# Performance work log

Hardware: AMD Instinct MI355X
Metric: run time of the kernel (lower is better)

## Reference

```python
import jax, jax.numpy as jnp
import numpy as np

B, S, D, H = 2, 2048, 1024, 16
DK = D // H


def setup_inputs() -> dict:
    key = jax.random.key(0)
    ks = jax.random.split(key, 7)
    scale = 1.0 / np.sqrt(D)
    return {
        "q": jax.random.normal(ks[0], (B, S, D), dtype=jnp.float32),
        "k": jax.random.normal(ks[1], (B, S, D), dtype=jnp.float32),
        "v": jax.random.normal(ks[2], (B, S, D), dtype=jnp.float32),
        "mask": jnp.ones((B, 1, 1, S), dtype=jnp.int32),
        "Wq": (jax.random.normal(ks[3], (D, D), dtype=jnp.float32) * scale),
        "Wk": (jax.random.normal(ks[4], (D, D), dtype=jnp.float32) * scale),
        "Wv": (jax.random.normal(ks[5], (D, D), dtype=jnp.float32) * scale),
        "Wo": (jax.random.normal(ks[6], (D, D), dtype=jnp.float32) * scale),
    }


def reference(q, k, v, mask, Wq, Wk, Wv, Wo):
    # nn.Linear(bias=False): y = x @ W.T
    def split_heads(x):  # [B,S,D] -> [B,H,S,DK]
        return x.reshape(B, S, H, DK).transpose(0, 2, 1, 3)

    qh = split_heads(q @ Wq.T)
    kh = split_heads(k @ Wk.T)
    vh = split_heads(v @ Wv.T)

    scores = jnp.einsum("bhqd,bhkd->bhqk", qh, kh) / jnp.sqrt(
        jnp.asarray(DK, dtype=qh.dtype))
    scores = jnp.where(mask == 0, jnp.asarray(-1e9, dtype=scores.dtype), scores)
    attn = jax.nn.softmax(scores, axis=-1)  # dropout p=0.0 -> identity

    ctx = jnp.einsum("bhqk,bhkd->bhqd", attn, vh)  # [B,H,S,DK]
    ctx = ctx.transpose(0, 2, 1, 3).reshape(B, S, D)
    return ctx @ Wo.T
```

## Files before the change

kernel.cpp:

```cpp
#include <hip/hip_runtime.h>


typedef __bf16 bf16x8 __attribute__((ext_vector_type(8)));
typedef __bf16 bf16x4 __attribute__((ext_vector_type(4)));
typedef float f32x4 __attribute__((ext_vector_type(4)));

#define B_ 2
#define S_ 2048
#define D_ 1024
#define H_ 16
#define DK_ 64
#define QSCALE 0.18033688011112042f

__global__ void detect_dtype(const unsigned int* __restrict__ qw,
                             int* __restrict__ flag) {
  int cnt = 0;
#pragma unroll
  for (int i = 0; i < 4; ++i) {
    unsigned int w = qw[threadIdx.x + 64 * i];
    int e = (w >> 7) & 0xFF;
    cnt += (e >= 100 && e <= 140) ? 1 : 0;
  }
#pragma unroll
  for (int off = 32; off > 0; off >>= 1) cnt += __shfl_down(cnt, off, 64);
  if (threadIdx.x == 0) *flag = (cnt >= 128) ? 0 : 1;
}

__device__ __forceinline__ bf16x8 load8cvt(const void* base, size_t eoff,
                                           bool f32) {
  if (!f32) return *(const bf16x8*)((const __bf16*)base + eoff);
  const float* p = (const float*)base + eoff;
  bf16x8 r;
#pragma unroll
  for (int j = 0; j < 8; ++j) r[j] = (__bf16)p[j];
  return r;
}

__device__ __forceinline__ void async_cp16(const __bf16* g, __bf16* l) {
  __builtin_amdgcn_global_load_lds(
      (const __attribute__((address_space(1))) unsigned int*)g,
      (__attribute__((address_space(3))) unsigned int*)l, 16, 0, 0);
}

template <int TM, int MODE>
__global__ __launch_bounds__(256) void gemmk(
    const void* X0, const void* X1, const void* X2,
    const void* W0, const void* W1, const void* W2,
    void* O0, void* O1, void* O2, const int* __restrict__ dflag) {
  constexpr int Kd = 1024, Nd = 1024;
  constexpr int NI = (TM == 128) ? 4 : 2;
  constexpr int ALOADS = TM / 64;
  const void* X = (blockIdx.z == 0) ? X0 : (blockIdx.z == 1 ? X1 : X2);
  const void* W = (blockIdx.z == 0) ? W0 : (blockIdx.z == 1 ? W1 : W2);
  void* O = (blockIdx.z == 0) ? O0 : (blockIdx.z == 1 ? O1 : O2);
  const bool f32io = (*dflag != 0);

  __shared__ __attribute__((aligned(16))) __bf16 As[TM * 32];
  __shared__ __attribute__((aligned(16))) __bf16 Bs[128 * 32];

  const int m0 = blockIdx.x * TM;
  const int n0 = blockIdx.y * 128;
  const int t = threadIdx.x;
  const int lane = t & 63, wave = t >> 6;
  const int l15 = lane & 15, quad = lane >> 4;
  const int wm = (TM == 128) ? (wave >> 1) * 64 : 0;
  const int wn = (TM == 128) ? (wave & 1) * 64 : wave * 32;

  const __bf16* gA[ALOADS];
  __bf16* ldsA[ALOADS];
#pragma unroll
  for (int i = 0; i < ALOADS; ++i) {
    int c = (wave * ALOADS + i) * 64 + lane;
    int row = c >> 2, j = c & 3;
    int jl = j ^ ((row >> 1) & 3);
    ldsA[i] = &As[(wave * ALOADS + i) * 512];
    if (MODE == 0) {
      gA[i] = (const __bf16*)X + (size_t)(m0 + row) * Kd + jl * 8;
    } else {
      int gm = m0 + row;
      gA[i] = (const __bf16*)X +
              (size_t)(gm >> 11) * (H_ * S_ * DK_) + (size_t)(gm & (S_ - 1)) * DK_ +
              jl * 8;
    }
  }
  const __bf16* gB[2];
  __bf16* ldsB[2];
#pragma unroll
  for (int i = 0; i < 2; ++i) {
    int c = (wave * 2 + i) * 64 + lane;
    int row = c >> 2, j = c & 3;
    int jl = j ^ ((row >> 1) & 3);
    ldsB[i] = &Bs[(wave * 2 + i) * 512];
    gB[i] = (const __bf16*)W + (size_t)(n0 + row) * Kd + jl * 8;
  }

  f32x4 acc[4][NI] = {};

  for (int k0 = 0; k0 < Kd; k0 += 32) {
    __syncthreads();
    if (!f32io) {
      if (MODE == 0) {
#pragma unroll
        for (int i = 0; i < ALOADS; ++i) async_cp16(gA[i] + k0, ldsA[i]);
      } else {
        const size_t koff = (size_t)(k0 >> 6) * (S_ * DK_) + (k0 & 32);
#pragma unroll
        for (int i = 0; i < ALOADS; ++i) async_cp16(gA[i] + koff, ldsA[i]);
      }
#pragma unroll
      for (int i = 0; i < 2; ++i) async_cp16(gB[i] + k0, ldsB[i]);
    } else {
#pragma unroll
      for (int i = 0; i < TM / 64; ++i) {
        int c = t + 256 * i;
        int row = c >> 2, j = c & 3;
        int jl = j ^ ((row >> 1) & 3);
        bf16x8 xv;
        if (MODE == 0) {
          xv = load8cvt(X, (size_t)(m0 + row) * Kd + k0 + jl * 8, true);
        } else {
          int gm = m0 + row, gk = k0 + jl * 8;
          xv = *(const bf16x8*)((const __bf16*)X +
                ((((size_t)(gm >> 11) * H_ + (gk >> 6)) * S_) +
                 (gm & (S_ - 1))) * DK_ + (gk & (DK_ - 1)));
        }
        *(bf16x8*)&As[row * 32 + j * 8] = xv;
      }
#pragma unroll
      for (int i = 0; i < 2; ++i) {
        int c = t + 256 * i;
        int row = c >> 2, j = c & 3;
        int jl = j ^ ((row >> 1) & 3);
        bf16x8 wv = load8cvt(W, (size_t)(n0 + row) * Kd + k0 + jl * 8, true);
        *(bf16x8*)&Bs[row * 32 + j * 8] = wv;
      }
    }
    __syncthreads();

    bf16x8 af[4], bfr[NI];
#pragma unroll
    for (int mi = 0; mi < 4; ++mi) {
      int row = wm + mi * 16 + l15;
      af[mi] = *(const bf16x8*)&As[row * 32 + ((quad ^ ((row >> 1) & 3)) << 3)];
    }
#pragma unroll
    for (int ni = 0; ni < NI; ++ni) {
      int row = wn + ni * 16 + l15;
      bfr[ni] = *(const bf16x8*)&Bs[row * 32 + ((quad ^ ((row >> 1) & 3)) << 3)];
    }
#pragma unroll
    for (int mi = 0; mi < 4; ++mi)
#pragma unroll
      for (int ni = 0; ni < NI; ++ni)
        acc[mi][ni] = __builtin_amdgcn_mfma_f32_16x16x32_bf16(af[mi], bfr[ni],
                                                              acc[mi][ni], 0, 0, 0);
  }

  const float oscale = (MODE == 0 && blockIdx.z == 0) ? QSCALE : 1.0f;
#pragma unroll
  for (int mi = 0; mi < 4; ++mi) {
#pragma unroll
    for (int ni = 0; ni < NI; ++ni) {
      int mbase = m0 + wm + mi * 16 + quad * 4;
      int n = n0 + wn + ni * 16 + l15;
      if (MODE == 0 && blockIdx.z == 2) {
        int b = mbase >> 11, sb = mbase & (S_ - 1);
        int h = n >> 6, dk = n & (DK_ - 1);
        bf16x4 pk;
#pragma unroll
        for (int r = 0; r < 4; ++r) pk[r] = (__bf16)acc[mi][ni][r];
        *(bf16x4*)&((__bf16*)O)[((size_t)(b * H_ + h) * DK_ + dk) * S_ + sb] = pk;
      } else {
#pragma unroll
        for (int r = 0; r < 4; ++r) {
          int m = mbase + r;
          float val = acc[mi][ni][r] * oscale;
          if (MODE == 0) {
            int b = m >> 11, s = m & (S_ - 1);
            int h = n >> 6, dk = n & (DK_ - 1);
            ((__bf16*)O)[((size_t)(b * H_ + h) * S_ + s) * DK_ + dk] = (__bf16)val;
          } else {
            size_t idx = (size_t)m * Nd + n;
            if (f32io) ((float*)O)[idx] = val;
            else       ((__bf16*)O)[idx] = (__bf16)val;
          }
        }
      }
    }
  }
}

__global__ __launch_bounds__(256) void attn(
    const __bf16* Qh, const __bf16* __restrict__ Kh,
    const __bf16* __restrict__ Vt, const int* __restrict__ mask,
    __bf16* Out) {
  __shared__ __attribute__((aligned(16))) __bf16 Ks[2][4096];
  __shared__ __attribute__((aligned(16))) __bf16 Vs[2][4096];
  __shared__ __attribute__((aligned(16))) __bf16 P[4][2048];

  const int t = threadIdx.x;
  const int lane = t & 63, wave = t >> 6;
  const int l15 = lane & 15, quad = lane >> 4;
  const int qb = blockIdx.x & 15;
  const int bh = blockIdx.x >> 4;
  const int b = bh >> 4;
  const int q0 = qb * 128 + wave * 32;

  const __bf16* Q = Qh + (size_t)bh * S_ * DK_;
  const __bf16* K = Kh + (size_t)bh * S_ * DK_;
  const __bf16* V = Vt + (size_t)bh * DK_ * S_;
  const int* mk = mask + b * S_;

  bf16x8 qf[2][2];
#pragma unroll
  for (int qt = 0; qt < 2; ++qt)
#pragma unroll
    for (int h = 0; h < 2; ++h)
      qf[qt][h] = *(const bf16x8*)&Q[(size_t)(q0 + qt * 16 + l15) * DK_ +
                                     h * 32 + quad * 8];

  f32x4 o[2][4] = {};
  float lsum[2][4] = {};

#pragma unroll
  for (int i = 0; i < 2; ++i) {
    int l = wave * 128 + i * 64 + lane;
    int row = l >> 3, jg = (l & 7) ^ (row & 7);
    async_cp16(K + (size_t)row * DK_ + jg * 8, &Ks[0][(size_t)(l - lane) * 8]);
    async_cp16(V + (size_t)row * S_ + jg * 8, &Vs[0][(size_t)(l - lane) * 8]);
  }
  __syncthreads();

  for (int kb = 0; kb < S_; kb += 64) {
    const int cur = (kb >> 6) & 1;
    if (kb + 64 < S_) {
#pragma unroll
      for (int i = 0; i < 2; ++i) {
        int l = wave * 128 + i * 64 + lane;
        int row = l >> 3, jg = (l & 7) ^ (row & 7);
        async_cp16(K + (size_t)(kb + 64 + row) * DK_ + jg * 8,
                   &Ks[cur ^ 1][(size_t)(l - lane) * 8]);
        async_cp16(V + (size_t)row * S_ + (kb + 64) + jg * 8,
                   &Vs[cur ^ 1][(size_t)(l - lane) * 8]);
      }
    }

    const __bf16* ks = &Ks[cur][0];
    f32x4 s[2][4];
#pragma unroll
    for (int tt = 0; tt < 4; ++tt) {
      int row = tt * 16 + l15;
      bf16x8 kf0 = *(const bf16x8*)&ks[row * 64 + ((quad ^ (l15 & 7)) << 3)];
      bf16x8 kf1 = *(const bf16x8*)&ks[row * 64 + (((4 + quad) ^ (l15 & 7)) << 3)];
#pragma unroll
      for (int qt = 0; qt < 2; ++qt) {
        f32x4 z = {};
        z = __builtin_amdgcn_mfma_f32_16x16x32_bf16(qf[qt][0], kf0, z, 0, 0, 0);
        z = __builtin_amdgcn_mfma_f32_16x16x32_bf16(qf[qt][1], kf1, z, 0, 0, 0);
        s[qt][tt] = z;
      }
    }

#pragma unroll
    for (int tt = 0; tt < 4; ++tt) {
      const int mv = mk[kb + tt * 16 + l15];
      const int jbase = tt * 2 + (l15 >> 3);
      const int kl = l15 & 7;
#pragma unroll
      for (int qt = 0; qt < 2; ++qt) {
#pragma unroll
        for (int r = 0; r < 4; ++r) {
          float e = mv ? __builtin_exp2f(s[qt][tt][r]) : 0.f;
          lsum[qt][r] += e;
          int qp = qt * 16 + quad * 4 + r;
          P[wave][qp * 64 + ((jbase ^ (qp & 7)) << 3) + kl] = (__bf16)e;
        }
      }
    }

    const __bf16* vs = &Vs[cur][0];
#pragma unroll
    for (int kt = 0; kt < 2; ++kt) {
      bf16x8 pf[2];
#pragma unroll
      for (int qt = 0; qt < 2; ++qt) {
        int qp = qt * 16 + l15;
        pf[qt] = *(const bf16x8*)&P[wave][qp * 64 +
                                          (((kt * 4 + quad) ^ (l15 & 7)) << 3)];
      }
#pragma unroll
      for (int nt = 0; nt < 4; ++nt) {
        int dk = nt * 16 + l15;
        bf16x8 vf = *(const bf16x8*)&vs[dk * 64 +
                                        (((kt * 4 + quad) ^ (l15 & 7)) << 3)];
#pragma unroll
        for (int qt = 0; qt < 2; ++qt)
          o[qt][nt] = __builtin_amdgcn_mfma_f32_16x16x32_bf16(pf[qt], vf,
                                                              o[qt][nt], 0, 0, 0);
      }
    }

    __syncthreads();
  }

  float rinv[2][4];
#pragma unroll
  for (int qt = 0; qt < 2; ++qt)
#pragma unroll
    for (int r = 0; r < 4; ++r) {
      float v = lsum[qt][r];
#pragma unroll
      for (int off = 8; off > 0; off >>= 1) v += __shfl_xor(v, off, 16);
      rinv[qt][r] = 1.0f / v;
    }

#pragma unroll
  for (int qt = 0; qt < 2; ++qt)
#pragma unroll
    for (int nt = 0; nt < 4; ++nt)
#pragma unroll
      for (int r = 0; r < 4; ++r) {
        int qrow = q0 + qt * 16 + quad * 4 + r;
        Out[(size_t)bh * S_ * DK_ + (size_t)qrow * DK_ + nt * 16 + l15] =
            (__bf16)(o[qt][nt][r] * rinv[qt][r]);
      }
}

extern "C" void kernel_launch(void* const* d_in, const int* in_sizes, int n_in,
                              void* d_out, int out_size, void* d_ws, size_t ws_size,
                              hipStream_t stream) {
  const void* q = d_in[0];
  const void* k = d_in[1];
  const void* v = d_in[2];
  const int* mask = (const int*)d_in[3];
  const void* Wq = d_in[4];
  const void* Wk = d_in[5];
  const void* Wv = d_in[6];
  const void* Wo = d_in[7];

  const size_t NE = (size_t)B_ * H_ * S_ * DK_;
  __bf16* Qh = (__bf16*)d_ws;
  __bf16* Kh = Qh + NE;
  int* dflag = (int*)((char*)d_ws + 2 * NE * sizeof(__bf16));
  __bf16* Vt = (__bf16*)d_out;

  detect_dtype<<<1, 64, 0, stream>>>((const unsigned int*)q, dflag);
  dim3 g1(32, 8, 3);
  gemmk<128, 0><<<g1, 256, 0, stream>>>(q, k, v, Wq, Wk, Wv, Qh, Kh, Vt, dflag);
  attn<<<512, 256, 0, stream>>>(Qh, Kh, Vt, mask, Qh);
  dim3 g2(64, 8, 1);
  gemmk<64, 1><<<g2, 256, 0, stream>>>(Qh, Qh, Qh, Wo, Wo, Wo, d_out, d_out,
                                       d_out, dflag);
}
```

Before: 265.6 us.

## Transpose MFMA operands for vectorized stores and compute softmax row sums via MFMA

The GEMM kernel swaps the A/B operands of its MFMAs on the non-transposed paths so each lane holds four consecutive output columns, which allows packed bf16x4/f32x4 stores instead of scalar ones. The attention kernel likewise computes the transposed output so stores are vectorized. It replaces the per-element softmax denominator accumulation and cross-lane shuffles with an extra MFMA against a ones vector over P. P-tile swizzle addresses are also precomputed. This trades some scalar adds and shuffles for extra MFMA work and computes the row sum from bf16-rounded P.

```diff
diff --git a/kernel.cpp b/kernel.cpp
--- a/kernel.cpp
+++ b/kernel.cpp
@@ -54,6 +54,7 @@
   const void* W = (blockIdx.z == 0) ? W0 : (blockIdx.z == 1 ? W1 : W2);
   void* O = (blockIdx.z == 0) ? O0 : (blockIdx.z == 1 ? O1 : O2);
   const bool f32io = (*dflag != 0);
+  const bool vt = (MODE == 0 && blockIdx.z == 2);
 
   __shared__ __attribute__((aligned(16))) __bf16 As[TM * 32];
   __shared__ __attribute__((aligned(16))) __bf16 Bs[128 * 32];
@@ -94,7 +95,7 @@
     gB[i] = (const __bf16*)W + (size_t)(n0 + row) * Kd + jl * 8;
   }
 
-  f32x4 acc[4][NI] = {};
+  f32x4 acc[4 * NI] = {};
 
   for (int k0 = 0; k0 < Kd; k0 += 32) {
     __syncthreads();
@@ -148,45 +149,65 @@
       int row = wn + ni * 16 + l15;
       bfr[ni] = *(const bf16x8*)&Bs[row * 32 + ((quad ^ ((row >> 1) & 3)) << 3)];
     }
+    if (vt) {
+#pragma unroll
+      for (int mi = 0; mi < 4; ++mi)
+#pragma unroll
+        for (int ni = 0; ni < NI; ++ni)
+          acc[mi * NI + ni] = __builtin_amdgcn_mfma_f32_16x16x32_bf16(
+              af[mi], bfr[ni], acc[mi * NI + ni], 0, 0, 0);
+    } else {
+#pragma unroll
+      for (int pi = 0; pi < NI; ++pi)
+#pragma unroll
+        for (int qi = 0; qi < 4; ++qi)
+          acc[pi * 4 + qi] = __builtin_amdgcn_mfma_f32_16x16x32_bf16(
+              bfr[pi], af[qi], acc[pi * 4 + qi], 0, 0, 0);
+    }
+  }
+
+  if (vt) {
 #pragma unroll
     for (int mi = 0; mi < 4; ++mi)
 #pragma unroll
-      for (int ni = 0; ni < NI; ++ni)
-        acc[mi][ni] = __builtin_amdgcn_mfma_f32_16x16x32_bf16(af[mi], bfr[ni],
-                                                              acc[mi][ni], 0, 0, 0);
-  }
-
-  const float oscale = (MODE == 0 && blockIdx.z == 0) ? QSCALE : 1.0f;
-#pragma unroll
-  for (int mi = 0; mi < 4; ++mi) {
-#pragma unroll
-    for (int ni = 0; ni < NI; ++ni) {
-      int mbase = m0 + wm + mi * 16 + quad * 4;
-      int n = n0 + wn + ni * 16 + l15;
-      if (MODE == 0 && blockIdx.z == 2) {
+      for (int ni = 0; ni < NI; ++ni) {
+        int mbase = m0 + wm + mi * 16 + quad * 4;
+        int n = n0 + wn + ni * 16 + l15;
         int b = mbase >> 11, sb = mbase & (S_ - 1);
         int h = n >> 6, dk = n & (DK_ - 1);
         bf16x4 pk;
 #pragma unroll
-        for (int r = 0; r < 4; ++r) pk[r] = (__bf16)acc[mi][ni][r];
+        for (int r = 0; r < 4; ++r) pk[r] = (__bf16)acc[mi * NI + ni][r];
         *(bf16x4*)&((__bf16*)O)[((size_t)(b * H_ + h) * DK_ + dk) * S_ + sb] = pk;
-      } else {
-#pragma unroll
-        for (int r = 0; r < 4; ++r) {
-          int m = mbase + r;
-          float val = acc[mi][ni][r] * oscale;
-          if (MODE == 0) {
-            int b = m >> 11, s = m & (S_ - 1);
-            int h = n >> 6, dk = n & (DK_ - 1);
-            ((__bf16*)O)[((size_t)(b * H_ + h) * S_ + s) * DK_ + dk] = (__bf16)val;
+      }
+  } else {
+    const float oscale = (MODE == 0 && blockIdx.z == 0) ? QSCALE : 1.0f;
+#pragma unroll
+    for (int pi = 0; pi < NI; ++pi)
+#pragma unroll
+      for (int qi = 0; qi < 4; ++qi) {
+        int nb = n0 + wn + pi * 16 + quad * 4;
+        int m = m0 + wm + qi * 16 + l15;
+        if (MODE == 0) {
+          int b = m >> 11, s = m & (S_ - 1);
+          int h = nb >> 6, dk = nb & (DK_ - 1);
+          bf16x4 pk;
+#pragma unroll
+          for (int r = 0; r < 4; ++r)
+            pk[r] = (__bf16)(acc[pi * 4 + qi][r] * oscale);
+          *(bf16x4*)&((__bf16*)O)[((size_t)(b * H_ + h) * S_ + s) * DK_ + dk] = pk;
+        } else {
+          size_t idx = (size_t)m * Nd + nb;
+          if (f32io) {
+            *(f32x4*)&((float*)O)[idx] = acc[pi * 4 + qi];
           } else {
-            size_t idx = (size_t)m * Nd + n;
-            if (f32io) ((float*)O)[idx] = val;
-            else       ((__bf16*)O)[idx] = (__bf16)val;
+            bf16x4 pk;
+#pragma unroll
+            for (int r = 0; r < 4; ++r) pk[r] = (__bf16)acc[pi * 4 + qi][r];
+            *(bf16x4*)&((__bf16*)O)[idx] = pk;
           }
         }
       }
-    }
   }
 }
 
@@ -219,8 +240,24 @@
       qf[qt][h] = *(const bf16x8*)&Q[(size_t)(q0 + qt * 16 + l15) * DK_ +
                                      h * 32 + quad * 8];
 
-  f32x4 o[2][4] = {};
-  float lsum[2][4] = {};
+  const int kl = l15 & 7, hb8 = l15 & 8;
+  int U[2][4], Wx[4];
+#pragma unroll
+  for (int qt = 0; qt < 2; ++qt)
+#pragma unroll
+    for (int r = 0; r < 4; ++r) {
+      int qp = qt * 16 + quad * 4 + r;
+      U[qt][r] = qp * 64 + kl + ((qp & 7) << 3);
+    }
+#pragma unroll
+  for (int tt = 0; tt < 4; ++tt) Wx[tt] = tt * 16 + hb8;
+
+  bf16x8 vones;
+#pragma unroll
+  for (int j = 0; j < 8; ++j) vones[j] = (__bf16)1.0f;
+
+  f32x4 oT[2][4] = {};
+  f32x4 lacc[2] = {};
 
 #pragma unroll
   for (int i = 0; i < 2; ++i) {
@@ -264,16 +301,12 @@
 #pragma unroll
     for (int tt = 0; tt < 4; ++tt) {
       const int mv = mk[kb + tt * 16 + l15];
-      const int jbase = tt * 2 + (l15 >> 3);
-      const int kl = l15 & 7;
 #pragma unroll
       for (int qt = 0; qt < 2; ++qt) {
 #pragma unroll
         for (int r = 0; r < 4; ++r) {
           float e = mv ? __builtin_exp2f(s[qt][tt][r]) : 0.f;
-          lsum[qt][r] += e;
-          int qp = qt * 16 + quad * 4 + r;
-          P[wave][qp * 64 + ((jbase ^ (qp & 7)) << 3) + kl] = (__bf16)e;
+          P[wave][U[qt][r] ^ Wx[tt]] = (__bf16)e;
         }
       }
     }
@@ -289,41 +322,36 @@
                                           (((kt * 4 + quad) ^ (l15 & 7)) << 3)];
       }
 #pragma unroll
+      for (int qt = 0; qt < 2; ++qt)
+        lacc[qt] = __builtin_amdgcn_mfma_f32_16x16x32_bf16(vones, pf[qt],
+                                                           lacc[qt], 0, 0, 0);
+#pragma unroll
       for (int nt = 0; nt < 4; ++nt) {
         int dk = nt * 16 + l15;
         bf16x8 vf = *(const bf16x8*)&vs[dk * 64 +
                                         (((kt * 4 + quad) ^ (l15 & 7)) << 3)];
 #pragma unroll
         for (int qt = 0; qt < 2; ++qt)
-          o[qt][nt] = __builtin_amdgcn_mfma_f32_16x16x32_bf16(pf[qt], vf,
-                                                              o[qt][nt], 0, 0, 0);
+          oT[qt][nt] = __builtin_amdgcn_mfma_f32_16x16x32_bf16(vf, pf[qt],
+                                                               oT[qt][nt], 0, 0, 0);
       }
     }
 
     __syncthreads();
   }
 
-  float rinv[2][4];
-#pragma unroll
-  for (int qt = 0; qt < 2; ++qt)
-#pragma unroll
-    for (int r = 0; r < 4; ++r) {
-      float v = lsum[qt][r];
-#pragma unroll
-      for (int off = 8; off > 0; off >>= 1) v += __shfl_xor(v, off, 16);
-      rinv[qt][r] = 1.0f / v;
-    }
-
-#pragma unroll
-  for (int qt = 0; qt < 2; ++qt)
-#pragma unroll
-    for (int nt = 0; nt < 4; ++nt)
-#pragma unroll
-      for (int r = 0; r < 4; ++r) {
-        int qrow = q0 + qt * 16 + quad * 4 + r;
-        Out[(size_t)bh * S_ * DK_ + (size_t)qrow * DK_ + nt * 16 + l15] =
-            (__bf16)(o[qt][nt][r] * rinv[qt][r]);
-      }
+#pragma unroll
+  for (int qt = 0; qt < 2; ++qt) {
+    float rinv = 1.0f / lacc[qt][0];
+    int q = q0 + qt * 16 + l15;
+#pragma unroll
+    for (int nt = 0; nt < 4; ++nt) {
+      bf16x4 pk;
+#pragma unroll
+      for (int r = 0; r < 4; ++r) pk[r] = (__bf16)(oT[qt][nt][r] * rinv);
+      *(bf16x4*)&Out[(size_t)bh * S_ * DK_ + (size_t)q * DK_ + nt * 16 + quad * 4] = pk;
+    }
+  }
 }
 
 extern "C" void kernel_launch(void* const* d_in, const int* in_sizes, int n_in,
```

Measured after the change: 296.9 us. 11.8% more time.

## Double GEMM k-tile, compute row sums via MFMA, and transpose attention output

Applied to the files above, without the earlier changes.

The projection GEMM now stages 64-wide K tiles with a matching 8-way XOR swizzle, which halves the number of loop iterations and barriers. In the attention kernel, the per-element softmax row-sum accumulation and the final cross-lane shuffle reduction are replaced by an extra MFMA against a vector of ones on the bf16 P fragments. The PV product is computed transposed (V as the A operand), so each lane holds contiguous dk values and can write packed bf16x4 stores. P-store addressing is precomputed with XOR offsets. The risks are larger LDS use per block and row sums now taken from bf16-rounded P rather than fp32 values.

```diff
diff --git a/kernel.cpp b/kernel.cpp
--- a/kernel.cpp
+++ b/kernel.cpp
@@ -49,14 +49,15 @@
     void* O0, void* O1, void* O2, const int* __restrict__ dflag) {
   constexpr int Kd = 1024, Nd = 1024;
   constexpr int NI = (TM == 128) ? 4 : 2;
-  constexpr int ALOADS = TM / 64;
+  constexpr int ACH = TM / 32;
+  constexpr int BCH = 4;
   const void* X = (blockIdx.z == 0) ? X0 : (blockIdx.z == 1 ? X1 : X2);
   const void* W = (blockIdx.z == 0) ? W0 : (blockIdx.z == 1 ? W1 : W2);
   void* O = (blockIdx.z == 0) ? O0 : (blockIdx.z == 1 ? O1 : O2);
   const bool f32io = (*dflag != 0);
 
-  __shared__ __attribute__((aligned(16))) __bf16 As[TM * 32];
-  __shared__ __attribute__((aligned(16))) __bf16 Bs[128 * 32];
+  __shared__ __attribute__((aligned(16))) __bf16 As[TM * 64];
+  __shared__ __attribute__((aligned(16))) __bf16 Bs[128 * 64];
 
   const int m0 = blockIdx.x * TM;
   const int n0 = blockIdx.y * 128;
@@ -66,55 +67,54 @@
   const int wm = (TM == 128) ? (wave >> 1) * 64 : 0;
   const int wn = (TM == 128) ? (wave & 1) * 64 : wave * 32;
 
-  const __bf16* gA[ALOADS];
-  __bf16* ldsA[ALOADS];
-#pragma unroll
-  for (int i = 0; i < ALOADS; ++i) {
-    int c = (wave * ALOADS + i) * 64 + lane;
-    int row = c >> 2, j = c & 3;
-    int jl = j ^ ((row >> 1) & 3);
-    ldsA[i] = &As[(wave * ALOADS + i) * 512];
+  const __bf16* gA[ACH];
+  __bf16* ldsA[ACH];
+#pragma unroll
+  for (int i = 0; i < ACH; ++i) {
+    int c = (wave * ACH + i) * 64 + lane;
+    int row = c >> 3, j = c & 7;
+    int jl = j ^ (row & 7);
+    ldsA[i] = &As[(wave * ACH + i) * 512];
     if (MODE == 0) {
       gA[i] = (const __bf16*)X + (size_t)(m0 + row) * Kd + jl * 8;
     } else {
       int gm = m0 + row;
-      gA[i] = (const __bf16*)X +
-              (size_t)(gm >> 11) * (H_ * S_ * DK_) + (size_t)(gm & (S_ - 1)) * DK_ +
-              jl * 8;
-    }
-  }
-  const __bf16* gB[2];
-  __bf16* ldsB[2];
-#pragma unroll
-  for (int i = 0; i < 2; ++i) {
-    int c = (wave * 2 + i) * 64 + lane;
-    int row = c >> 2, j = c & 3;
-    int jl = j ^ ((row >> 1) & 3);
-    ldsB[i] = &Bs[(wave * 2 + i) * 512];
+      gA[i] = (const __bf16*)X + (size_t)(gm >> 11) * (H_ * S_ * DK_) +
+              (size_t)(gm & (S_ - 1)) * DK_ + jl * 8;
+    }
+  }
+  const __bf16* gB[BCH];
+  __bf16* ldsB[BCH];
+#pragma unroll
+  for (int i = 0; i < BCH; ++i) {
+    int c = (wave * BCH + i) * 64 + lane;
+    int row = c >> 3, j = c & 7;
+    int jl = j ^ (row & 7);
+    ldsB[i] = &Bs[(wave * BCH + i) * 512];
     gB[i] = (const __bf16*)W + (size_t)(n0 + row) * Kd + jl * 8;
   }
 
   f32x4 acc[4][NI] = {};
 
-  for (int k0 = 0; k0 < Kd; k0 += 32) {
+  for (int k0 = 0; k0 < Kd; k0 += 64) {
     __syncthreads();
     if (!f32io) {
       if (MODE == 0) {
 #pragma unroll
-        for (int i = 0; i < ALOADS; ++i) async_cp16(gA[i] + k0, ldsA[i]);
+        for (int i = 0; i < ACH; ++i) async_cp16(gA[i] + k0, ldsA[i]);
       } else {
-        const size_t koff = (size_t)(k0 >> 6) * (S_ * DK_) + (k0 & 32);
-#pragma unroll
-        for (int i = 0; i < ALOADS; ++i) async_cp16(gA[i] + koff, ldsA[i]);
-      }
-#pragma unroll
-      for (int i = 0; i < 2; ++i) async_cp16(gB[i] + k0, ldsB[i]);
+        const size_t koff = (size_t)(k0 >> 6) * (S_ * DK_);
+#pragma unroll
+        for (int i = 0; i < ACH; ++i) async_cp16(gA[i] + koff, ldsA[i]);
+      }
+#pragma unroll
+      for (int i = 0; i < BCH; ++i) async_cp16(gB[i] + k0, ldsB[i]);
     } else {
 #pragma unroll
-      for (int i = 0; i < TM / 64; ++i) {
+      for (int i = 0; i < TM / 32; ++i) {
         int c = t + 256 * i;
-        int row = c >> 2, j = c & 3;
-        int jl = j ^ ((row >> 1) & 3);
+        int row = c >> 3, j = c & 7;
+        int jl = j ^ (row & 7);
         bf16x8 xv;
         if (MODE == 0) {
           xv = load8cvt(X, (size_t)(m0 + row) * Kd + k0 + jl * 8, true);
@@ -124,36 +124,41 @@
                 ((((size_t)(gm >> 11) * H_ + (gk >> 6)) * S_) +
                  (gm & (S_ - 1))) * DK_ + (gk & (DK_ - 1)));
         }
-        *(bf16x8*)&As[row * 32 + j * 8] = xv;
-      }
-#pragma unroll
-      for (int i = 0; i < 2; ++i) {
+        *(bf16x8*)&As[row * 64 + j * 8] = xv;
+      }
+#pragma unroll
+      for (int i = 0; i < 4; ++i) {
         int c = t + 256 * i;
-        int row = c >> 2, j = c & 3;
-        int jl = j ^ ((row >> 1) & 3);
+        int row = c >> 3, j = c & 7;
+        int jl = j ^ (row & 7);
         bf16x8 wv = load8cvt(W, (size_t)(n0 + row) * Kd + k0 + jl * 8, true);
-        *(bf16x8*)&Bs[row * 32 + j * 8] = wv;
+        *(bf16x8*)&Bs[row * 64 + j * 8] = wv;
       }
     }
     __syncthreads();
 
-    bf16x8 af[4], bfr[NI];
-#pragma unroll
-    for (int mi = 0; mi < 4; ++mi) {
-      int row = wm + mi * 16 + l15;
-      af[mi] = *(const bf16x8*)&As[row * 32 + ((quad ^ ((row >> 1) & 3)) << 3)];
-    }
-#pragma unroll
-    for (int ni = 0; ni < NI; ++ni) {
-      int row = wn + ni * 16 + l15;
-      bfr[ni] = *(const bf16x8*)&Bs[row * 32 + ((quad ^ ((row >> 1) & 3)) << 3)];
-    }
-#pragma unroll
-    for (int mi = 0; mi < 4; ++mi)
-#pragma unroll
-      for (int ni = 0; ni < NI; ++ni)
-        acc[mi][ni] = __builtin_amdgcn_mfma_f32_16x16x32_bf16(af[mi], bfr[ni],
-                                                              acc[mi][ni], 0, 0, 0);
+#pragma unroll
+    for (int h = 0; h < 2; ++h) {
+      bf16x8 af[4], bfr[NI];
+#pragma unroll
+      for (int mi = 0; mi < 4; ++mi) {
+        int row = wm + mi * 16 + l15;
+        af[mi] = *(const bf16x8*)&As[row * 64 +
+                                     (((h * 4 + quad) ^ (row & 7)) << 3)];
+      }
+#pragma unroll
+      for (int ni = 0; ni < NI; ++ni) {
+        int row = wn + ni * 16 + l15;
+        bfr[ni] = *(const bf16x8*)&Bs[row * 64 +
+                                      (((h * 4 + quad) ^ (row & 7)) << 3)];
+      }
+#pragma unroll
+      for (int mi = 0; mi < 4; ++mi)
+#pragma unroll
+        for (int ni = 0; ni < NI; ++ni)
+          acc[mi][ni] = __builtin_amdgcn_mfma_f32_16x16x32_bf16(
+              af[mi], bfr[ni], acc[mi][ni], 0, 0, 0);
+    }
   }
 
   const float oscale = (MODE == 0 && blockIdx.z == 0) ? QSCALE : 1.0f;
@@ -219,8 +224,24 @@
       qf[qt][h] = *(const bf16x8*)&Q[(size_t)(q0 + qt * 16 + l15) * DK_ +
                                      h * 32 + quad * 8];
 
-  f32x4 o[2][4] = {};
-  float lsum[2][4] = {};
+  const int kl = l15 & 7, hb8 = l15 & 8;
+  int U[2][4], Wx[4];
+#pragma unroll
+  for (int qt = 0; qt < 2; ++qt)
+#pragma unroll
+    for (int r = 0; r < 4; ++r) {
+      int qp = qt * 16 + quad * 4 + r;
+      U[qt][r] = qp * 64 + kl + ((qp & 7) << 3);
+    }
+#pragma unroll
+  for (int tt = 0; tt < 4; ++tt) Wx[tt] = tt * 16 + hb8;
+
+  bf16x8 vones;
+#pragma unroll
+  for (int j = 0; j < 8; ++j) vones[j] = (__bf16)1.0f;
+
+  f32x4 oT[2][4] = {};
+  f32x4 lacc[2] = {};
 
 #pragma unroll
   for (int i = 0; i < 2; ++i) {
@@ -264,16 +285,12 @@
 #pragma unroll
     for (int tt = 0; tt < 4; ++tt) {
       const int mv = mk[kb + tt * 16 + l15];
-      const int jbase = tt * 2 + (l15 >> 3);
-      const int kl = l15 & 7;
 #pragma unroll
       for (int qt = 0; qt < 2; ++qt) {
 #pragma unroll
         for (int r = 0; r < 4; ++r) {
           float e = mv ? __builtin_exp2f(s[qt][tt][r]) : 0.f;
-          lsum[qt][r] += e;
-          int qp = qt * 16 + quad * 4 + r;
-          P[wave][qp * 64 + ((jbase ^ (qp & 7)) << 3) + kl] = (__bf16)e;
+          P[wave][U[qt][r] ^ Wx[tt]] = (__bf16)e;
         }
       }
     }
@@ -289,41 +306,36 @@
                                           (((kt * 4 + quad) ^ (l15 & 7)) << 3)];
       }
 #pragma unroll
+      for (int qt = 0; qt < 2; ++qt)
+        lacc[qt] = __builtin_amdgcn_mfma_f32_16x16x32_bf16(vones, pf[qt],
+                                                           lacc[qt], 0, 0, 0);
+#pragma unroll
       for (int nt = 0; nt < 4; ++nt) {
         int dk = nt * 16 + l15;
         bf16x8 vf = *(const bf16x8*)&vs[dk * 64 +
                                         (((kt * 4 + quad) ^ (l15 & 7)) << 3)];
 #pragma unroll
         for (int qt = 0; qt < 2; ++qt)
-          o[qt][nt] = __builtin_amdgcn_mfma_f32_16x16x32_bf16(pf[qt], vf,
-                                                              o[qt][nt], 0, 0, 0);
+          oT[qt][nt] = __builtin_amdgcn_mfma_f32_16x16x32_bf16(vf, pf[qt],
+                                                               oT[qt][nt], 0, 0, 0);
       }
     }
 
     __syncthreads();
   }
 
-  float rinv[2][4];
-#pragma unroll
-  for (int qt = 0; qt < 2; ++qt)
-#pragma unroll
-    for (int r = 0; r < 4; ++r) {
-      float v = lsum[qt][r];
-#pragma unroll
-      for (int off = 8; off > 0; off >>= 1) v += __shfl_xor(v, off, 16);
-      rinv[qt][r] = 1.0f / v;
-    }
-
-#pragma unroll
-  for (int qt = 0; qt < 2; ++qt)
-#pragma unroll
-    for (int nt = 0; nt < 4; ++nt)
-#pragma unroll
-      for (int r = 0; r < 4; ++r) {
-        int qrow = q0 + qt * 16 + quad * 4 + r;
-        Out[(size_t)bh * S_ * DK_ + (size_t)qrow * DK_ + nt * 16 + l15] =
-            (__bf16)(o[qt][nt][r] * rinv[qt][r]);
-      }
+#pragma unroll
+  for (int qt = 0; qt < 2; ++qt) {
+    float rinv = 1.0f / lacc[qt][0];
+    int q = q0 + qt * 16 + l15;
+#pragma unroll
+    for (int nt = 0; nt < 4; ++nt) {
+      bf16x4 pk;
+#pragma unroll
+      for (int r = 0; r < 4; ++r) pk[r] = (__bf16)(oT[qt][nt][r] * rinv);
+      *(bf16x4*)&Out[(size_t)bh * S_ * DK_ + (size_t)q * DK_ + nt * 16 + quad * 4] = pk;
+    }
+  }
 }
 
 extern "C" void kernel_launch(void* const* d_in, const int* in_sizes, int n_in,
```

After: 269.1 us. Within noise of the previous version (+1.3%).
